# Optimization experiments

Measured on AMD Instinct MI355X. Metric: run time of the kernel, lower is better.

## Reference

```python
import jax, jax.numpy as jnp
import numpy as np

N = 100000
E = 3200000
NODE_IN = 118
D = 32
H = 4
C = D // H  # 8
EDGE_DIM = 50 + 3
L = 4
LN_EPS = 1e-5


def _layernorm(x, g, b):
    mu = jnp.mean(x, axis=-1, keepdims=True)
    var = jnp.mean(jnp.square(x - mu), axis=-1, keepdims=True)
    return (x - mu) * jax.lax.rsqrt(var + LN_EPS) * g + b


def setup_inputs() -> dict:
    key = jax.random.key(0)
    ks = jax.random.split(key, 20)
    x = jax.random.normal(ks[0], (N, NODE_IN), dtype=jnp.float32)
    edge_index = jax.random.randint(ks[1], (2, E), 0, N, dtype=jnp.int32)
    edge_len = jax.random.normal(ks[2], (E, 50), dtype=jnp.float32)
    edge_vec = jax.random.normal(ks[3], (E, 3), dtype=jnp.float32)
    s_in = 1.0 / np.sqrt(NODE_IN)
    s_d = 1.0 / np.sqrt(D)
    s_e = 1.0 / np.sqrt(EDGE_DIM)
    node_in_W = jax.random.normal(ks[4], (NODE_IN, D), dtype=jnp.float32) * s_in
    node_in_b = jnp.zeros((D,), dtype=jnp.float32)
    ln_g = jnp.ones((L, D), dtype=jnp.float32)
    ln_b = jnp.zeros((L, D), dtype=jnp.float32)
    Wq = jax.random.normal(ks[5], (L, D, D), dtype=jnp.float32) * s_d
    bq = jnp.zeros((L, D), dtype=jnp.float32)
    Wk = jax.random.normal(ks[6], (L, D, D), dtype=jnp.float32) * s_d
    bk = jnp.zeros((L, D), dtype=jnp.float32)
    Wv = jax.random.normal(ks[7], (L, D, D), dtype=jnp.float32) * s_d
    bv = jnp.zeros((L, D), dtype=jnp.float32)
    We = jax.random.normal(ks[8], (L, EDGE_DIM, D), dtype=jnp.float32) * s_e  # lin_edge, bias=False
    Wskip = jax.random.normal(ks[9], (L, D, D), dtype=jnp.float32) * s_d
    bskip = jnp.zeros((L, D), dtype=jnp.float32)
    return {"x": x, "edge_index": edge_index, "edge_len": edge_len, "edge_vec": edge_vec,
            "node_in_W": node_in_W, "node_in_b": node_in_b, "ln_g": ln_g, "ln_b": ln_b,
            "Wq": Wq, "bq": bq, "Wk": Wk, "bk": bk, "Wv": Wv, "bv": bv,
            "We": We, "Wskip": Wskip, "bskip": bskip}


def reference(x, edge_index, edge_len, edge_vec, node_in_W, node_in_b, ln_g, ln_b,
              Wq, bq, Wk, bk, Wv, bv, We, Wskip, bskip):
    src = edge_index[0]  # j (source), messages flow source -> target
    dst = edge_index[1]  # i (target), softmax grouped by dst
    ef = jnp.concatenate([edge_len, edge_vec], axis=-1)  # [E, 53]
    h = x @ node_in_W + node_in_b  # [N, D]
    scale = 1.0 / np.sqrt(C)
    for l in range(L):
        xn = _layernorm(h, ln_g[l], ln_b[l])
        q = (xn @ Wq[l] + bq[l]).reshape(N, H, C)
        k = (xn @ Wk[l] + bk[l]).reshape(N, H, C)
        v = (xn @ Wv[l] + bv[l]).reshape(N, H, C)
        e = (ef @ We[l]).reshape(E, H, C)  # per-edge key/value shift
        kj = k[src] + e                     # [E, H, C]
        alpha = jnp.sum(q[dst] * kj, axis=-1) * scale  # [E, H]
        # segment softmax over incoming edges of each target node
        amax = jax.ops.segment_max(alpha, dst, num_segments=N)  # [N, H]
        amax = jnp.where(jnp.isfinite(amax), amax, 0.0)
        ex = jnp.exp(alpha - amax[dst])
        denom = jax.ops.segment_sum(ex, dst, num_segments=N)
        w = ex / (denom[dst] + 1e-16)       # [E, H]
        msg = (v[src] + e) * w[:, :, None]  # [E, H, C]
        agg = jax.ops.segment_sum(msg.reshape(E, H * C), dst, num_segments=N)  # [N, D]
        y = agg + xn @ Wskip[l] + bskip[l]  # concat heads + root skip (lin_skip(x_i))
        h = h + y                            # residual
    return h
```

## Files before the change

### kernel.cpp

```cpp
#include <hip/hip_runtime.h>
#include <hip/hip_bf16.h>
#include <math.h>

#define N_NODES 100000
#define N_EDGES 3200000
#define NODE_IN 118
#define DIM 32
#define EDF 53
#define NLAYER 4

typedef __attribute__((ext_vector_type(8))) short short8;
typedef __attribute__((ext_vector_type(4))) short short4v;
typedef __attribute__((ext_vector_type(4))) float f32x4;
typedef unsigned short u16;
typedef unsigned int u32;

static __device__ __forceinline__ float bfhi2f(u32 hi) {
    union { u32 i; float f; } x; x.i = hi; return x.f;
}
static __device__ __forceinline__ u16 f2bf(float f) {
    union { float f; u32 i; } x; x.f = f;
    u32 i = x.i;
    return (u16)((i + 0x7FFFu + ((i >> 16) & 1u)) >> 16);
}

__global__ __launch_bounds__(256) void k_count(const int* __restrict__ dst, int* __restrict__ cnt) {
    int e = blockIdx.x * 256 + threadIdx.x;
    atomicAdd(&cnt[dst[e]], 1);
}

__global__ __launch_bounds__(256) void k_scanA(const int* __restrict__ cnt, int* __restrict__ off,
                                               int* __restrict__ bsum) {
    __shared__ int s[256];
    int t = threadIdx.x; int i = blockIdx.x * 256 + t;
    int v = (i < N_NODES) ? cnt[i] : 0;
    s[t] = v; __syncthreads();
    for (int d = 1; d < 256; d <<= 1) {
        int x = (t >= d) ? s[t - d] : 0; __syncthreads();
        s[t] += x; __syncthreads();
    }
    if (i < N_NODES) off[i] = s[t] - v;
    if (t == 255) bsum[blockIdx.x] = s[t];
}

__global__ __launch_bounds__(512) void k_scanB(int* bsum, int nb) {
    __shared__ int s[512];
    int t = threadIdx.x;
    int v = (t < nb) ? bsum[t] : 0;
    s[t] = v; __syncthreads();
    for (int d = 1; d < 512; d <<= 1) {
        int x = (t >= d) ? s[t - d] : 0; __syncthreads();
        s[t] += x; __syncthreads();
    }
    if (t < nb) bsum[t] = s[t] - v;
}

__global__ __launch_bounds__(256) void k_scanC(int* off, const int* __restrict__ bsum) {
    int i = blockIdx.x * 256 + threadIdx.x;
    if (i < N_NODES) off[i] += bsum[blockIdx.x];
    if (i == 0) off[N_NODES] = N_EDGES;
}

__global__ __launch_bounds__(256) void k_fill(const int* __restrict__ src, const int* __restrict__ dst,
                                              const int* __restrict__ off, int* __restrict__ cur,
                                              int* __restrict__ eidp, int* __restrict__ esrc) {
    int e = blockIdx.x * 256 + threadIdx.x;
    int d = dst[e];
    int p = off[d] + atomicAdd(&cur[d], 1);
    eidp[p] = e; esrc[p] = src[e];
}

__global__ __launch_bounds__(256) void k_init(const float* __restrict__ x, const float* __restrict__ W,
                                              const float* __restrict__ b, float* __restrict__ h) {
    __shared__ float Ws[NODE_IN * DIM];
    __shared__ float xs[8][NODE_IN];
    int t = threadIdx.x;
    for (int i = t; i < NODE_IN * DIM; i += 256) Ws[i] = W[i];
    int nb = blockIdx.x * 8;
    for (int i = t; i < 8 * NODE_IN; i += 256) {
        int n = i / NODE_IN, j = i % NODE_IN;
        xs[n][j] = x[(size_t)(nb + n) * NODE_IN + j];
    }
    __syncthreads();
    int n = t >> 5, c = t & 31;
    float acc = b[c];
    #pragma unroll 2
    for (int j = 0; j < NODE_IN; j++) acc += xs[n][j] * Ws[j * DIM + c];
    h[(size_t)(nb + n) * DIM + c] = acc;
}

template <int NL>
__global__ __launch_bounds__(256) void k_egemm(const float* __restrict__ elen, const float* __restrict__ evec,
                                               const int* __restrict__ eidp, const float* __restrict__ We,
                                               u16* __restrict__ eout) {
    int tid = threadIdx.x;
    int lane = tid & 63;
    int wv = (blockIdx.x * 256 + tid) >> 6;
    int nw = (gridDim.x * 256) >> 6;
    int n15 = lane & 15, kb = lane >> 4;

    short8 bf[2][2 * NL];
    for (int s = 0; s < 2; s++) {
        for (int t = 0; t < 2 * NL; t++) {
            int n = t * 16 + n15;
            int lay = n >> 5, c = n & 31;
            short8 tmp;
            #pragma unroll
            for (int j = 0; j < 8; j++) {
                int kk = s * 32 + kb * 8 + j;
                float w = (kk < EDF) ? We[(size_t)lay * EDF * DIM + (size_t)kk * DIM + c] : 0.f;
                ((u16*)&tmp)[j] = f2bf(w);
            }
            bf[s][t] = tmp;
        }
    }

    const int NT = N_EDGES / 16;

    auto LOADA = [&](int tile, float* fv) {
        int pos = tile * 16 + n15;
        int eid = eidp[pos];
        const float* lp = elen + (size_t)eid * 50;
        {
            const float2* p2 = (const float2*)(lp + kb * 8);
            #pragma unroll
            for (int j = 0; j < 4; j++) { float2 t2 = p2[j]; fv[2 * j] = t2.x; fv[2 * j + 1] = t2.y; }
        }
        if (kb < 2) {
            const float2* p2 = (const float2*)(lp + 32 + kb * 8);
            #pragma unroll
            for (int j = 0; j < 4; j++) { float2 t2 = p2[j]; fv[8 + 2 * j] = t2.x; fv[8 + 2 * j + 1] = t2.y; }
        } else if (kb == 2) {
            float2 t2 = *(const float2*)(lp + 48);
            const float* vp = evec + (size_t)eid * 3;
            fv[8] = t2.x; fv[9] = t2.y; fv[10] = vp[0]; fv[11] = vp[1]; fv[12] = vp[2];
            fv[13] = 0.f; fv[14] = 0.f; fv[15] = 0.f;
        } else {
            #pragma unroll
            for (int j = 8; j < 16; j++) fv[j] = 0.f;
        }
    };

    float cur[16];
    if (wv < NT) LOADA(wv, cur);

    for (int tile = wv; tile < NT; tile += nw) {
        int nxt = tile + nw;
        float nx[16];
        if (nxt < NT) LOADA(nxt, nx);

        short8 af[2];
        #pragma unroll
        for (int s = 0; s < 2; s++) {
            short8 tmp;
            #pragma unroll
            for (int j = 0; j < 8; j++) ((u16*)&tmp)[j] = f2bf(cur[s * 8 + j]);
            af[s] = tmp;
        }

        size_t pos = (size_t)tile * 16 + n15;
        #pragma unroll
        for (int t = 0; t < 2 * NL; t++) {
            f32x4 z = {0.f, 0.f, 0.f, 0.f};
            z = __builtin_amdgcn_mfma_f32_16x16x32_bf16(bf[0][t], af[0], z, 0, 0, 0);
            z = __builtin_amdgcn_mfma_f32_16x16x32_bf16(bf[1][t], af[1], z, 0, 0, 0);
            int lay = t >> 1;
            int ch = (t & 1) * 16 + kb * 4;
            short4v sv;
            #pragma unroll
            for (int r = 0; r < 4; r++) ((u16*)&sv)[r] = f2bf(z[r]);
            *(short4v*)&eout[((size_t)lay * N_EDGES + pos) * DIM + ch] = sv;
        }

        #pragma unroll
        for (int j = 0; j < 16; j++) cur[j] = nx[j];
    }
}

__global__ __launch_bounds__(256) void k_node(const float* __restrict__ h,
        const float* __restrict__ g, const float* __restrict__ bta,
        const float* __restrict__ Wq, const float* __restrict__ bq,
        const float* __restrict__ Wk, const float* __restrict__ bk,
        const float* __restrict__ Wv, const float* __restrict__ bv,
        const float* __restrict__ Ws, const float* __restrict__ bs,
        float* __restrict__ qo, float* __restrict__ ko, float* __restrict__ vo, float* __restrict__ so) {
    __shared__ float WQ[DIM * DIM], WK[DIM * DIM], WV[DIM * DIM], WS[DIM * DIM];
    __shared__ float xn[8][DIM];
    int t = threadIdx.x;
    for (int i = t; i < DIM * DIM; i += 256) { WQ[i] = Wq[i]; WK[i] = Wk[i]; WV[i] = Wv[i]; WS[i] = Ws[i]; }
    int n = t >> 5, c = t & 31;
    size_t node = (size_t)blockIdx.x * 8 + n;
    float hv = h[node * DIM + c];
    float s1 = hv;
    for (int d = 1; d < 32; d <<= 1) s1 += __shfl_xor(s1, d, 64);
    float mu = s1 * (1.f / 32.f);
    float dv = hv - mu;
    float s2 = dv * dv;
    for (int d = 1; d < 32; d <<= 1) s2 += __shfl_xor(s2, d, 64);
    float inv = rsqrtf(s2 * (1.f / 32.f) + 1e-5f);
    float xv = dv * inv * g[c] + bta[c];
    xn[n][c] = xv;
    __syncthreads();
    float aq = bq[c], ak = bk[c], av = bv[c], as = bs[c];
    #pragma unroll 4
    for (int j = 0; j < DIM; j++) {
        float xj = xn[n][j];
        aq += xj * WQ[j * DIM + c];
        ak += xj * WK[j * DIM + c];
        av += xj * WV[j * DIM + c];
        as += xj * WS[j * DIM + c];
    }
    size_t o = node * DIM + c;
    qo[o] = aq; ko[o] = ak; vo[o] = av; so[o] = as;
}

__global__ __launch_bounds__(256) void k_aggr(const int* __restrict__ off, const int* __restrict__ esrc,
        const u16* __restrict__ eb,
        const float* __restrict__ qb, const float* __restrict__ kb, const float* __restrict__ vb,
        const float* __restrict__ h, const float* __restrict__ sk, float* __restrict__ out) {
    int tid = threadIdx.x;
    size_t node = (size_t)blockIdx.x * 4 + (tid >> 6);
    int lane = tid & 63;
    int eg = lane >> 3, cq = lane & 7, c0 = cq * 4;
    float4 qv = *(const float4*)&qb[node * DIM + c0];
    int o0 = off[node], o1 = off[node + 1];
    float4 nacc = {0.f, 0.f, 0.f, 0.f};
    float dacc = 0.f;
    const float scale = 0.35355339059327373f;
    for (int p0 = o0; p0 < o1; p0 += 8) {
        int p = p0 + eg;
        bool act = p < o1;
        int pc = act ? p : o0;
        int sj = esrc[pc];
        uint2 ebv = *(const uint2*)&eb[(size_t)pc * DIM + c0];
        float4 kv = *(const float4*)&kb[(size_t)sj * DIM + c0];
        float4 vv = *(const float4*)&vb[(size_t)sj * DIM + c0];
        float e0 = bfhi2f(ebv.x << 16), e1 = bfhi2f(ebv.x & 0xFFFF0000u);
        float e2 = bfhi2f(ebv.y << 16), e3 = bfhi2f(ebv.y & 0xFFFF0000u);
        float a = qv.x * (kv.x + e0);
        a = fmaf(qv.y, kv.y + e1, a);
        a = fmaf(qv.z, kv.z + e2, a);
        a = fmaf(qv.w, kv.w + e3, a);
        a += __shfl_xor(a, 1);
        float ex = act ? __expf(a * scale) : 0.f;
        nacc.x = fmaf(ex, vv.x + e0, nacc.x);
        nacc.y = fmaf(ex, vv.y + e1, nacc.y);
        nacc.z = fmaf(ex, vv.z + e2, nacc.z);
        nacc.w = fmaf(ex, vv.w + e3, nacc.w);
        dacc += ex;
    }
    #pragma unroll
    for (int d = 8; d < 64; d <<= 1) {
        nacc.x += __shfl_xor(nacc.x, d);
        nacc.y += __shfl_xor(nacc.y, d);
        nacc.z += __shfl_xor(nacc.z, d);
        nacc.w += __shfl_xor(nacc.w, d);
        dacc   += __shfl_xor(dacc, d);
    }
    if (eg == 0) {
        float inv = 1.f / (dacc + 1e-16f);
        float4 hv = *(const float4*)&h[node * DIM + c0];
        float4 sv = *(const float4*)&sk[node * DIM + c0];
        float4 o;
        o.x = hv.x + nacc.x * inv + sv.x;
        o.y = hv.y + nacc.y * inv + sv.y;
        o.z = hv.z + nacc.z * inv + sv.z;
        o.w = hv.w + nacc.w * inv + sv.w;
        *(float4*)&out[node * DIM + c0] = o;
    }
}

extern "C" void kernel_launch(void* const* d_in, const int* in_sizes, int n_in,
                              void* d_out, int out_size, void* d_ws, size_t ws_size,
                              hipStream_t stream) {
    const float* x    = (const float*)d_in[0];
    const int*   ei   = (const int*)d_in[1];
    const int*   src  = ei;
    const int*   dst  = ei + N_EDGES;
    const float* elen = (const float*)d_in[2];
    const float* evec = (const float*)d_in[3];
    const float* niW  = (const float*)d_in[4];
    const float* nib  = (const float*)d_in[5];
    const float* lng  = (const float*)d_in[6];
    const float* lnb  = (const float*)d_in[7];
    const float* Wq   = (const float*)d_in[8];
    const float* bq   = (const float*)d_in[9];
    const float* Wk   = (const float*)d_in[10];
    const float* bk   = (const float*)d_in[11];
    const float* Wv   = (const float*)d_in[12];
    const float* bv   = (const float*)d_in[13];
    const float* We   = (const float*)d_in[14];
    const float* Wsk  = (const float*)d_in[15];
    const float* bsk  = (const float*)d_in[16];
    float* out = (float*)d_out;

    unsigned char* w = (unsigned char*)d_ws;
    auto alloc = [&](size_t bytes) -> void* {
        void* p = (void*)w; w += (bytes + 255) & ~(size_t)255; return p;
    };
    int*   off  = (int*)alloc((N_NODES + 1) * sizeof(int));
    int*   cnt  = (int*)alloc(N_NODES * sizeof(int));
    int*   bsum = (int*)alloc(512 * sizeof(int));
    int*   eidp = (int*)alloc((size_t)N_EDGES * sizeof(int));
    int*   esrc = (int*)alloc((size_t)N_EDGES * sizeof(int));
    float* h    = (float*)alloc((size_t)N_NODES * DIM * sizeof(float));
    float* qb   = (float*)alloc((size_t)N_NODES * DIM * sizeof(float));
    float* kb   = (float*)alloc((size_t)N_NODES * DIM * sizeof(float));
    float* vb   = (float*)alloc((size_t)N_NODES * DIM * sizeof(float));
    float* skb  = (float*)alloc((size_t)N_NODES * DIM * sizeof(float));
    size_t used = (size_t)(w - (unsigned char*)d_ws);
    size_t e_full = (size_t)NLAYER * N_EDGES * DIM * sizeof(u16);
    size_t e_one  = (size_t)N_EDGES * DIM * sizeof(u16);
    bool full = (used + e_full) <= ws_size;
    u16* ebuf = (u16*)alloc(full ? e_full : e_one);

    const int EB = N_EDGES / 256;
    const int NB = N_NODES / 8;
    const int AB = N_NODES / 4;
    const int nbScan = (N_NODES + 255) / 256;

    hipMemsetAsync(cnt, 0, N_NODES * sizeof(int), stream);
    k_count<<<EB, 256, 0, stream>>>(dst, cnt);
    k_scanA<<<nbScan, 256, 0, stream>>>(cnt, off, bsum);
    k_scanB<<<1, 512, 0, stream>>>(bsum, nbScan);
    k_scanC<<<nbScan, 256, 0, stream>>>(off, bsum);
    hipMemsetAsync(cnt, 0, N_NODES * sizeof(int), stream);
    k_fill<<<EB, 256, 0, stream>>>(src, dst, off, cnt, eidp, esrc);

    k_init<<<NB, 256, 0, stream>>>(x, niW, nib, h);

    if (full) k_egemm<4><<<4096, 256, 0, stream>>>(elen, evec, eidp, We, ebuf);

    for (int l = 0; l < NLAYER; l++) {
        if (!full) k_egemm<1><<<4096, 256, 0, stream>>>(elen, evec, eidp, We + (size_t)l * EDF * DIM, ebuf);
        k_node<<<NB, 256, 0, stream>>>(h, lng + l * DIM, lnb + l * DIM,
                                       Wq + (size_t)l * DIM * DIM, bq + l * DIM,
                                       Wk + (size_t)l * DIM * DIM, bk + l * DIM,
                                       Wv + (size_t)l * DIM * DIM, bv + l * DIM,
                                       Wsk + (size_t)l * DIM * DIM, bsk + l * DIM,
                                       qb, kb, vb, skb);
        const u16* el = full ? (ebuf + (size_t)l * N_EDGES * DIM) : ebuf;
        k_aggr<<<AB, 256, 0, stream>>>(off, esrc, el, qb, kb, vb, h, skb,
                                       (l == NLAYER - 1) ? out : h);
    }
}
```

Measured before the change: 1.567 ms.

## Read edge features sequentially and scatter outputs by rank; software-pipeline aggregation loads

The fill kernel now records each edge's CSR position (rank) instead of a permutation array. The edge GEMM then reads edge_len/edge_vec coalesced in original order and scatters its bf16 outputs to the sorted position, replacing a gathered 200-byte read per edge with a scattered 64-byte write. The aggregation kernel prefetches the next edge's source index and k/v/e values one iteration ahead and folds the softmax scale into q. This adds register pressure and scattered writes in exchange for fewer gathered reads and better latency hiding.

```diff
diff --git a/kernel.cpp b/kernel.cpp
--- a/kernel.cpp
+++ b/kernel.cpp
@@ -63,11 +63,12 @@
 
 __global__ __launch_bounds__(256) void k_fill(const int* __restrict__ src, const int* __restrict__ dst,
                                               const int* __restrict__ off, int* __restrict__ cur,
-                                              int* __restrict__ eidp, int* __restrict__ esrc) {
+                                              int* __restrict__ rank, int* __restrict__ esrc) {
     int e = blockIdx.x * 256 + threadIdx.x;
     int d = dst[e];
     int p = off[d] + atomicAdd(&cur[d], 1);
-    eidp[p] = e; esrc[p] = src[e];
+    rank[e] = p;
+    esrc[p] = src[e];
 }
 
 __global__ __launch_bounds__(256) void k_init(const float* __restrict__ x, const float* __restrict__ W,
@@ -91,7 +92,7 @@
 
 template <int NL>
 __global__ __launch_bounds__(256) void k_egemm(const float* __restrict__ elen, const float* __restrict__ evec,
-                                               const int* __restrict__ eidp, const float* __restrict__ We,
+                                               const int* __restrict__ rank, const float* __restrict__ We,
                                                u16* __restrict__ eout) {
     int tid = threadIdx.x;
     int lane = tid & 63;
@@ -117,10 +118,10 @@
 
     const int NT = N_EDGES / 16;
 
-    auto LOADA = [&](int tile, float* fv) {
+    auto LOADA = [&](int tile, float* fv, int& rk) {
         int pos = tile * 16 + n15;
-        int eid = eidp[pos];
-        const float* lp = elen + (size_t)eid * 50;
+        rk = rank[pos];
+        const float* lp = elen + (size_t)pos * 50;
         {
             const float2* p2 = (const float2*)(lp + kb * 8);
             #pragma unroll
@@ -132,7 +133,7 @@
             for (int j = 0; j < 4; j++) { float2 t2 = p2[j]; fv[8 + 2 * j] = t2.x; fv[8 + 2 * j + 1] = t2.y; }
         } else if (kb == 2) {
             float2 t2 = *(const float2*)(lp + 48);
-            const float* vp = evec + (size_t)eid * 3;
+            const float* vp = evec + (size_t)pos * 3;
             fv[8] = t2.x; fv[9] = t2.y; fv[10] = vp[0]; fv[11] = vp[1]; fv[12] = vp[2];
             fv[13] = 0.f; fv[14] = 0.f; fv[15] = 0.f;
         } else {
@@ -141,13 +142,13 @@
         }
     };
 
-    float cur[16];
-    if (wv < NT) LOADA(wv, cur);
+    float cur[16]; int rkc = 0;
+    if (wv < NT) LOADA(wv, cur, rkc);
 
     for (int tile = wv; tile < NT; tile += nw) {
         int nxt = tile + nw;
-        float nx[16];
-        if (nxt < NT) LOADA(nxt, nx);
+        float nx[16]; int rkn = rkc;
+        if (nxt < NT) LOADA(nxt, nx, rkn);
 
         short8 af[2];
         #pragma unroll
@@ -158,7 +159,7 @@
             af[s] = tmp;
         }
 
-        size_t pos = (size_t)tile * 16 + n15;
+        size_t rowbase = (size_t)rkc * DIM;
         #pragma unroll
         for (int t = 0; t < 2 * NL; t++) {
             f32x4 z = {0.f, 0.f, 0.f, 0.f};
@@ -169,11 +170,12 @@
             short4v sv;
             #pragma unroll
             for (int r = 0; r < 4; r++) ((u16*)&sv)[r] = f2bf(z[r]);
-            *(short4v*)&eout[((size_t)lay * N_EDGES + pos) * DIM + ch] = sv;
+            *(short4v*)&eout[(size_t)lay * N_EDGES * DIM + rowbase + ch] = sv;
         }
 
         #pragma unroll
         for (int j = 0; j < 16; j++) cur[j] = nx[j];
+        rkc = rkn;
     }
 }
 
@@ -222,32 +224,47 @@
     size_t node = (size_t)blockIdx.x * 4 + (tid >> 6);
     int lane = tid & 63;
     int eg = lane >> 3, cq = lane & 7, c0 = cq * 4;
+    const float scale = 0.35355339059327373f;
     float4 qv = *(const float4*)&qb[node * DIM + c0];
+    qv.x *= scale; qv.y *= scale; qv.z *= scale; qv.w *= scale;
     int o0 = off[node], o1 = off[node + 1];
     float4 nacc = {0.f, 0.f, 0.f, 0.f};
     float dacc = 0.f;
-    const float scale = 0.35355339059327373f;
+
+    int p1 = o0 + eg;
+    bool a1 = p1 < o1; int pc1 = a1 ? p1 : o0;
+    int sj1 = esrc[pc1];
+    uint2 eb1 = *(const uint2*)&eb[(size_t)pc1 * DIM + c0];
+    float4 kv1 = *(const float4*)&kb[(size_t)sj1 * DIM + c0];
+    float4 vv1 = *(const float4*)&vb[(size_t)sj1 * DIM + c0];
+    int p2 = p1 + 8;
+    bool a2 = p2 < o1; int pc2 = a2 ? p2 : o0;
+    int sj2 = esrc[pc2];
+
     for (int p0 = o0; p0 < o1; p0 += 8) {
-        int p = p0 + eg;
-        bool act = p < o1;
-        int pc = act ? p : o0;
-        int sj = esrc[pc];
-        uint2 ebv = *(const uint2*)&eb[(size_t)pc * DIM + c0];
-        float4 kv = *(const float4*)&kb[(size_t)sj * DIM + c0];
-        float4 vv = *(const float4*)&vb[(size_t)sj * DIM + c0];
-        float e0 = bfhi2f(ebv.x << 16), e1 = bfhi2f(ebv.x & 0xFFFF0000u);
-        float e2 = bfhi2f(ebv.y << 16), e3 = bfhi2f(ebv.y & 0xFFFF0000u);
-        float a = qv.x * (kv.x + e0);
-        a = fmaf(qv.y, kv.y + e1, a);
-        a = fmaf(qv.z, kv.z + e2, a);
-        a = fmaf(qv.w, kv.w + e3, a);
+        uint2 ebn = *(const uint2*)&eb[(size_t)pc2 * DIM + c0];
+        float4 kvn = *(const float4*)&kb[(size_t)sj2 * DIM + c0];
+        float4 vvn = *(const float4*)&vb[(size_t)sj2 * DIM + c0];
+        int p3 = p2 + 8;
+        bool a3 = p3 < o1; int pc3 = a3 ? p3 : o0;
+        int sj3 = esrc[pc3];
+
+        float e0 = bfhi2f(eb1.x << 16), e1 = bfhi2f(eb1.x & 0xFFFF0000u);
+        float e2 = bfhi2f(eb1.y << 16), e3 = bfhi2f(eb1.y & 0xFFFF0000u);
+        float a = qv.x * (kv1.x + e0);
+        a = fmaf(qv.y, kv1.y + e1, a);
+        a = fmaf(qv.z, kv1.z + e2, a);
+        a = fmaf(qv.w, kv1.w + e3, a);
         a += __shfl_xor(a, 1);
-        float ex = act ? __expf(a * scale) : 0.f;
-        nacc.x = fmaf(ex, vv.x + e0, nacc.x);
-        nacc.y = fmaf(ex, vv.y + e1, nacc.y);
-        nacc.z = fmaf(ex, vv.z + e2, nacc.z);
-        nacc.w = fmaf(ex, vv.w + e3, nacc.w);
+        float ex = a1 ? __expf(a) : 0.f;
+        nacc.x = fmaf(ex, vv1.x + e0, nacc.x);
+        nacc.y = fmaf(ex, vv1.y + e1, nacc.y);
+        nacc.z = fmaf(ex, vv1.z + e2, nacc.z);
+        nacc.w = fmaf(ex, vv1.w + e3, nacc.w);
         dacc += ex;
+
+        a1 = a2; eb1 = ebn; kv1 = kvn; vv1 = vvn;
+        a2 = a3; pc2 = pc3; sj2 = sj3; p2 = p3;
     }
     #pragma unroll
     for (int d = 8; d < 64; d <<= 1) {
@@ -301,7 +318,7 @@
     int*   off  = (int*)alloc((N_NODES + 1) * sizeof(int));
     int*   cnt  = (int*)alloc(N_NODES * sizeof(int));
     int*   bsum = (int*)alloc(512 * sizeof(int));
-    int*   eidp = (int*)alloc((size_t)N_EDGES * sizeof(int));
+    int*   rank = (int*)alloc((size_t)N_EDGES * sizeof(int));
     int*   esrc = (int*)alloc((size_t)N_EDGES * sizeof(int));
     float* h    = (float*)alloc((size_t)N_NODES * DIM * sizeof(float));
     float* qb   = (float*)alloc((size_t)N_NODES * DIM * sizeof(float));
@@ -325,14 +342,14 @@
     k_scanB<<<1, 512, 0, stream>>>(bsum, nbScan);
     k_scanC<<<nbScan, 256, 0, stream>>>(off, bsum);
     hipMemsetAsync(cnt, 0, N_NODES * sizeof(int), stream);
-    k_fill<<<EB, 256, 0, stream>>>(src, dst, off, cnt, eidp, esrc);
+    k_fill<<<EB, 256, 0, stream>>>(src, dst, off, cnt, rank, esrc);
 
     k_init<<<NB, 256, 0, stream>>>(x, niW, nib, h);
 
-    if (full) k_egemm<4><<<4096, 256, 0, stream>>>(elen, evec, eidp, We, ebuf);
+    if (full) k_egemm<4><<<4096, 256, 0, stream>>>(elen, evec, rank, We, ebuf);
 
     for (int l = 0; l < NLAYER; l++) {
-        if (!full) k_egemm<1><<<4096, 256, 0, stream>>>(elen, evec, eidp, We + (size_t)l * EDF * DIM, ebuf);
+        if (!full) k_egemm<1><<<4096, 256, 0, stream>>>(elen, evec, rank, We + (size_t)l * EDF * DIM, ebuf);
         k_node<<<NB, 256, 0, stream>>>(h, lng + l * DIM, lnb + l * DIM,
                                        Wq + (size_t)l * DIM * DIM, bq + l * DIM,
                                        Wk + (size_t)l * DIM * DIM, bk + l * DIM,
```

Measured after the change: 1.590 ms. About the same (+1.4%).

## Store edge features in original order, bf16 K/V, and prefetch gathers in aggregation

Applied to the files above, without the earlier changes.

The edge GEMM now reads edge features sequentially in original edge order instead of gathering them through the CSR permutation. Its output is stored in original order, so the aggregation kernel now gathers it by edge id. K and V are stored as bf16 to halve gather bandwidth, and the attention scale is folded into Q. The residual and skip terms are pre-summed in the node kernel. The aggregation loop is software-pipelined with a two-deep prefetch of indices and gathered rows. This trades a scattered read in the GEMM for a scattered read in the aggregation, and adds bf16 rounding on K and V.

```diff
diff --git a/kernel.cpp b/kernel.cpp
--- a/kernel.cpp
+++ b/kernel.cpp
@@ -63,11 +63,12 @@
 
 __global__ __launch_bounds__(256) void k_fill(const int* __restrict__ src, const int* __restrict__ dst,
                                               const int* __restrict__ off, int* __restrict__ cur,
-                                              int* __restrict__ eidp, int* __restrict__ esrc) {
+                                              int* __restrict__ eidx, int* __restrict__ esrc) {
     int e = blockIdx.x * 256 + threadIdx.x;
     int d = dst[e];
     int p = off[d] + atomicAdd(&cur[d], 1);
-    eidp[p] = e; esrc[p] = src[e];
+    eidx[p] = e;
+    esrc[p] = src[e];
 }
 
 __global__ __launch_bounds__(256) void k_init(const float* __restrict__ x, const float* __restrict__ W,
@@ -91,8 +92,7 @@
 
 template <int NL>
 __global__ __launch_bounds__(256) void k_egemm(const float* __restrict__ elen, const float* __restrict__ evec,
-                                               const int* __restrict__ eidp, const float* __restrict__ We,
-                                               u16* __restrict__ eout) {
+                                               const float* __restrict__ We, u16* __restrict__ eout) {
     int tid = threadIdx.x;
     int lane = tid & 63;
     int wv = (blockIdx.x * 256 + tid) >> 6;
@@ -119,8 +119,7 @@
 
     auto LOADA = [&](int tile, float* fv) {
         int pos = tile * 16 + n15;
-        int eid = eidp[pos];
-        const float* lp = elen + (size_t)eid * 50;
+        const float* lp = elen + (size_t)pos * 50;
         {
             const float2* p2 = (const float2*)(lp + kb * 8);
             #pragma unroll
@@ -132,7 +131,7 @@
             for (int j = 0; j < 4; j++) { float2 t2 = p2[j]; fv[8 + 2 * j] = t2.x; fv[8 + 2 * j + 1] = t2.y; }
         } else if (kb == 2) {
             float2 t2 = *(const float2*)(lp + 48);
-            const float* vp = evec + (size_t)eid * 3;
+            const float* vp = evec + (size_t)pos * 3;
             fv[8] = t2.x; fv[9] = t2.y; fv[10] = vp[0]; fv[11] = vp[1]; fv[12] = vp[2];
             fv[13] = 0.f; fv[14] = 0.f; fv[15] = 0.f;
         } else {
@@ -158,7 +157,7 @@
             af[s] = tmp;
         }
 
-        size_t pos = (size_t)tile * 16 + n15;
+        size_t rowbase = ((size_t)tile * 16 + n15) * DIM;
         #pragma unroll
         for (int t = 0; t < 2 * NL; t++) {
             f32x4 z = {0.f, 0.f, 0.f, 0.f};
@@ -169,7 +168,7 @@
             short4v sv;
             #pragma unroll
             for (int r = 0; r < 4; r++) ((u16*)&sv)[r] = f2bf(z[r]);
-            *(short4v*)&eout[((size_t)lay * N_EDGES + pos) * DIM + ch] = sv;
+            *(short4v*)&eout[(size_t)lay * N_EDGES * DIM + rowbase + ch] = sv;
         }
 
         #pragma unroll
@@ -183,7 +182,7 @@
         const float* __restrict__ Wk, const float* __restrict__ bk,
         const float* __restrict__ Wv, const float* __restrict__ bv,
         const float* __restrict__ Ws, const float* __restrict__ bs,
-        float* __restrict__ qo, float* __restrict__ ko, float* __restrict__ vo, float* __restrict__ so) {
+        float* __restrict__ qo, u16* __restrict__ ko, u16* __restrict__ vo, float* __restrict__ hso) {
     __shared__ float WQ[DIM * DIM], WK[DIM * DIM], WV[DIM * DIM], WS[DIM * DIM];
     __shared__ float xn[8][DIM];
     int t = threadIdx.x;
@@ -211,13 +210,16 @@
         as += xj * WS[j * DIM + c];
     }
     size_t o = node * DIM + c;
-    qo[o] = aq; ko[o] = ak; vo[o] = av; so[o] = as;
-}
-
-__global__ __launch_bounds__(256) void k_aggr(const int* __restrict__ off, const int* __restrict__ esrc,
-        const u16* __restrict__ eb,
-        const float* __restrict__ qb, const float* __restrict__ kb, const float* __restrict__ vb,
-        const float* __restrict__ h, const float* __restrict__ sk, float* __restrict__ out) {
+    qo[o] = aq * 0.35355339059327373f;
+    ko[o] = f2bf(ak);
+    vo[o] = f2bf(av);
+    hso[o] = hv + as;
+}
+
+__global__ __launch_bounds__(256) void k_aggr(const int* __restrict__ off, const int* __restrict__ eidx,
+        const int* __restrict__ esrc, const u16* __restrict__ eb,
+        const float* __restrict__ qb, const u16* __restrict__ kb, const u16* __restrict__ vb,
+        const float* __restrict__ hs, float* __restrict__ out) {
     int tid = threadIdx.x;
     size_t node = (size_t)blockIdx.x * 4 + (tid >> 6);
     int lane = tid & 63;
@@ -226,28 +228,49 @@
     int o0 = off[node], o1 = off[node + 1];
     float4 nacc = {0.f, 0.f, 0.f, 0.f};
     float dacc = 0.f;
-    const float scale = 0.35355339059327373f;
-    for (int p0 = o0; p0 < o1; p0 += 8) {
-        int p = p0 + eg;
-        bool act = p < o1;
-        int pc = act ? p : o0;
-        int sj = esrc[pc];
-        uint2 ebv = *(const uint2*)&eb[(size_t)pc * DIM + c0];
-        float4 kv = *(const float4*)&kb[(size_t)sj * DIM + c0];
-        float4 vv = *(const float4*)&vb[(size_t)sj * DIM + c0];
-        float e0 = bfhi2f(ebv.x << 16), e1 = bfhi2f(ebv.x & 0xFFFF0000u);
-        float e2 = bfhi2f(ebv.y << 16), e3 = bfhi2f(ebv.y & 0xFFFF0000u);
-        float a = qv.x * (kv.x + e0);
-        a = fmaf(qv.y, kv.y + e1, a);
-        a = fmaf(qv.z, kv.z + e2, a);
-        a = fmaf(qv.w, kv.w + e3, a);
+
+    int pA = o0 + eg;  bool aA = pA < o1; int qAi = aA ? pA : o0;
+    int eA = eidx[qAi], sA = esrc[qAi];
+    int pB = pA + 8;   bool aB = pB < o1; int qBi = aB ? pB : o0;
+    int eB = eidx[qBi], sB = esrc[qBi];
+    int pC = pB + 8;   bool aC = pC < o1; int qCi = aC ? pC : o0;
+    int eC = eidx[qCi], sC = esrc[qCi];
+
+    uint2 dAe = *(const uint2*)&eb[(size_t)eA * DIM + c0];
+    uint2 dAk = *(const uint2*)&kb[(size_t)sA * DIM + c0];
+    uint2 dAv = *(const uint2*)&vb[(size_t)sA * DIM + c0];
+    uint2 dBe = *(const uint2*)&eb[(size_t)eB * DIM + c0];
+    uint2 dBk = *(const uint2*)&kb[(size_t)sB * DIM + c0];
+    uint2 dBv = *(const uint2*)&vb[(size_t)sB * DIM + c0];
+
+    for (int p = o0; p < o1; p += 8) {
+        uint2 dCe = *(const uint2*)&eb[(size_t)eC * DIM + c0];
+        uint2 dCk = *(const uint2*)&kb[(size_t)sC * DIM + c0];
+        uint2 dCv = *(const uint2*)&vb[(size_t)sC * DIM + c0];
+        int pD = pC + 8; bool aD = pD < o1; int qDi = aD ? pD : o0;
+        int eD = eidx[qDi], sD = esrc[qDi];
+
+        float e0 = bfhi2f(dAe.x << 16), e1 = bfhi2f(dAe.x & 0xFFFF0000u);
+        float e2 = bfhi2f(dAe.y << 16), e3 = bfhi2f(dAe.y & 0xFFFF0000u);
+        float k0 = bfhi2f(dAk.x << 16), k1 = bfhi2f(dAk.x & 0xFFFF0000u);
+        float k2 = bfhi2f(dAk.y << 16), k3 = bfhi2f(dAk.y & 0xFFFF0000u);
+        float v0 = bfhi2f(dAv.x << 16), v1 = bfhi2f(dAv.x & 0xFFFF0000u);
+        float v2 = bfhi2f(dAv.y << 16), v3 = bfhi2f(dAv.y & 0xFFFF0000u);
+        float a = qv.x * (k0 + e0);
+        a = fmaf(qv.y, k1 + e1, a);
+        a = fmaf(qv.z, k2 + e2, a);
+        a = fmaf(qv.w, k3 + e3, a);
         a += __shfl_xor(a, 1);
-        float ex = act ? __expf(a * scale) : 0.f;
-        nacc.x = fmaf(ex, vv.x + e0, nacc.x);
-        nacc.y = fmaf(ex, vv.y + e1, nacc.y);
-        nacc.z = fmaf(ex, vv.z + e2, nacc.z);
-        nacc.w = fmaf(ex, vv.w + e3, nacc.w);
+        float ex = aA ? __expf(a) : 0.f;
+        nacc.x = fmaf(ex, v0 + e0, nacc.x);
+        nacc.y = fmaf(ex, v1 + e1, nacc.y);
+        nacc.z = fmaf(ex, v2 + e2, nacc.z);
+        nacc.w = fmaf(ex, v3 + e3, nacc.w);
         dacc += ex;
+
+        aA = aB; dAe = dBe; dAk = dBk; dAv = dBv;
+        aB = aC; dBe = dCe; dBk = dCk; dBv = dCv;
+        aC = aD; eC = eD; sC = sD; pC = pD;
     }
     #pragma unroll
     for (int d = 8; d < 64; d <<= 1) {
@@ -259,13 +282,12 @@
     }
     if (eg == 0) {
         float inv = 1.f / (dacc + 1e-16f);
-        float4 hv = *(const float4*)&h[node * DIM + c0];
-        float4 sv = *(const float4*)&sk[node * DIM + c0];
+        float4 hv = *(const float4*)&hs[node * DIM + c0];
         float4 o;
-        o.x = hv.x + nacc.x * inv + sv.x;
-        o.y = hv.y + nacc.y * inv + sv.y;
-        o.z = hv.z + nacc.z * inv + sv.z;
-        o.w = hv.w + nacc.w * inv + sv.w;
+        o.x = hv.x + nacc.x * inv;
+        o.y = hv.y + nacc.y * inv;
+        o.z = hv.z + nacc.z * inv;
+        o.w = hv.w + nacc.w * inv;
         *(float4*)&out[node * DIM + c0] = o;
     }
 }
@@ -301,13 +323,13 @@
     int*   off  = (int*)alloc((N_NODES + 1) * sizeof(int));
     int*   cnt  = (int*)alloc(N_NODES * sizeof(int));
     int*   bsum = (int*)alloc(512 * sizeof(int));
-    int*   eidp = (int*)alloc((size_t)N_EDGES * sizeof(int));
+    int*   eidx = (int*)alloc((size_t)N_EDGES * sizeof(int));
     int*   esrc = (int*)alloc((size_t)N_EDGES * sizeof(int));
     float* h    = (float*)alloc((size_t)N_NODES * DIM * sizeof(float));
     float* qb   = (float*)alloc((size_t)N_NODES * DIM * sizeof(float));
-    float* kb   = (float*)alloc((size_t)N_NODES * DIM * sizeof(float));
-    float* vb   = (float*)alloc((size_t)N_NODES * DIM * sizeof(float));
-    float* skb  = (float*)alloc((size_t)N_NODES * DIM * sizeof(float));
+    u16*   kb   = (u16*)alloc((size_t)N_NODES * DIM * sizeof(u16));
+    u16*   vb   = (u16*)alloc((size_t)N_NODES * DIM * sizeof(u16));
+    float* hsb  = (float*)alloc((size_t)N_NODES * DIM * sizeof(float));
     size_t used = (size_t)(w - (unsigned char*)d_ws);
     size_t e_full = (size_t)NLAYER * N_EDGES * DIM * sizeof(u16);
     size_t e_one  = (size_t)N_EDGES * DIM * sizeof(u16);
@@ -325,22 +347,22 @@
     k_scanB<<<1, 512, 0, stream>>>(bsum, nbScan);
     k_scanC<<<nbScan, 256, 0, stream>>>(off, bsum);
     hipMemsetAsync(cnt, 0, N_NODES * sizeof(int), stream);
-    k_fill<<<EB, 256, 0, stream>>>(src, dst, off, cnt, eidp, esrc);
+    k_fill<<<EB, 256, 0, stream>>>(src, dst, off, cnt, eidx, esrc);
 
     k_init<<<NB, 256, 0, stream>>>(x, niW, nib, h);
 
-    if (full) k_egemm<4><<<4096, 256, 0, stream>>>(elen, evec, eidp, We, ebuf);
+    if (full) k_egemm<4><<<4096, 256, 0, stream>>>(elen, evec, We, ebuf);
 
     for (int l = 0; l < NLAYER; l++) {
-        if (!full) k_egemm<1><<<4096, 256, 0, stream>>>(elen, evec, eidp, We + (size_t)l * EDF * DIM, ebuf);
+        if (!full) k_egemm<1><<<4096, 256, 0, stream>>>(elen, evec, We + (size_t)l * EDF * DIM, ebuf);
         k_node<<<NB, 256, 0, stream>>>(h, lng + l * DIM, lnb + l * DIM,
                                        Wq + (size_t)l * DIM * DIM, bq + l * DIM,
                                        Wk + (size_t)l * DIM * DIM, bk + l * DIM,
                                        Wv + (size_t)l * DIM * DIM, bv + l * DIM,
                                        Wsk + (size_t)l * DIM * DIM, bsk + l * DIM,
-                                       qb, kb, vb, skb);
+                                       qb, kb, vb, hsb);
         const u16* el = full ? (ebuf + (size_t)l * N_EDGES * DIM) : ebuf;
-        k_aggr<<<AB, 256, 0, stream>>>(off, esrc, el, qb, kb, vb, h, skb,
+        k_aggr<<<AB, 256, 0, stream>>>(off, eidx, esrc, el, qb, kb, vb, hsb,
                                        (l == NLAYER - 1) ? out : h);
     }
 }
```

New measurement: 1.574 ms. Within noise of the previous version (+0.4%).
